# Optimization experiments

Hardware: AMD Instinct MI355X
Metric: run time of the kernel (lower is better)

Reference implementation:

```python
import jax, jax.numpy as jnp
import numpy as np

N = 100000   # nodes
E = 1600000  # edges (avg degree 16)
D = 256      # in_channels == out_channels
EPS = 1e-3   # Keras LayerNormalization default epsilon


def setup_inputs() -> dict:
    key = jax.random.key(0)
    k1, k2, k3 = jax.random.split(key, 3)
    x = jax.random.normal(k1, (N, D), dtype=jnp.float32)
    edge_index = jax.random.randint(k2, (2, E), 0, N, dtype=jnp.int32)
    W = jax.random.normal(k3, (D, D), dtype=jnp.float32) / np.float32(np.sqrt(D))
    b = jnp.zeros((D,), dtype=jnp.float32)
    gamma = jnp.ones((D,), dtype=jnp.float32)
    beta = jnp.zeros((D,), dtype=jnp.float32)
    return {"x": x, "edge_index": edge_index, "W": W, "b": b, "gamma": gamma, "beta": beta}


def reference(x, edge_index, W, b, gamma, beta):
    src, dst = edge_index[0], edge_index[1]
    n = x.shape[0]
    # in-degree with self-loop, symmetric GCN normalization 1/sqrt(d_i d_j)
    deg = jax.ops.segment_sum(jnp.ones((src.shape[0],), x.dtype), dst, num_segments=n) + 1.0
    norm = jax.lax.rsqrt(deg)               # [N]
    h = x @ W                               # [N, D] dense transform
    msg = h[src] * norm[src, None]          # gather + scale, [E, D]
    agg = jax.ops.segment_sum(msg, dst, num_segments=n) * norm[:, None]
    agg = agg + h * (norm * norm)[:, None] + b   # self-loop term + bias
    # residual (in_channels == out_channels) + layer norm
    y = x + agg
    mean = jnp.mean(y, axis=-1, keepdims=True)
    var = jnp.mean(jnp.square(y - mean), axis=-1, keepdims=True)
    return gamma * (y - mean) * jax.lax.rsqrt(var + EPS) + beta
```

## Files before the change

kernel.cpp:

```cpp
#include <hip/hip_runtime.h>


#define D_DIM 256
#define NPART 8
#define SLOTS 64

typedef __attribute__((ext_vector_type(8))) short short8;
typedef __attribute__((ext_vector_type(4))) float f32x4;
typedef __attribute__((ext_vector_type(2))) float f32x2;

__device__ __forceinline__ unsigned short f2bf(float f) {
    unsigned int u = __builtin_bit_cast(unsigned int, f);
    u = (u + 0x7fffu + ((u >> 16) & 1u)) >> 16;
    return (unsigned short)u;
}
__device__ __forceinline__ unsigned int pack2(float a, float b) {
    return (unsigned int)f2bf(a) | ((unsigned int)f2bf(b) << 16);
}

__device__ __forceinline__ unsigned int fp8e(float f) {
    float a = fminf(fmaxf(f, -448.f), 448.f);
    unsigned int u = __builtin_bit_cast(unsigned int, a);
    unsigned int s = (u >> 24) & 0x80u;
    int e = (int)((u >> 23) & 0xffu);
    unsigned int man = u & 0x7fffffu;
    if (e >= 121) {
        unsigned int mant = man >> 20;
        unsigned int rest = man & 0xfffffu;
        unsigned int inc = (rest > 0x80000u) || (rest == 0x80000u && (mant & 1u));
        unsigned int code = (((unsigned int)(e - 120)) << 3) | mant;
        code += inc;
        if (code > 0x7eu) code = 0x7eu;
        return s | code;
    }
    float m = fabsf(a) * 512.f;
    unsigned int mi = (unsigned int)rintf(m);
    return s | mi;
}

__global__ void zero_ints(int* __restrict__ p, int n) {
    int i = blockIdx.x * blockDim.x + threadIdx.x;
    if (i < n) p[i] = 0;
}

__global__ void fill_pad_part(const int* __restrict__ src, const int* __restrict__ dst,
                              int E, int* __restrict__ cnt, int* __restrict__ srcs_pad,
                              int npp) {
    const int part = blockIdx.x & (NPART - 1);
    const int bid  = blockIdx.x >> 3;
    const int nblk = gridDim.x >> 3;
    const int lo = part * npp, hi = lo + npp;
    for (int e = bid * blockDim.x + threadIdx.x; e < E; e += nblk * blockDim.x) {
        int d = dst[e];
        if (d >= lo && d < hi) {
            int pos = atomicAdd(&cnt[d], 1);
            if (pos < SLOTS) srcs_pad[(size_t)d * SLOTS + pos] = src[e];
        }
    }
}

__global__ void make_nrm(const int* __restrict__ cnt, float* __restrict__ nrm, int N) {
    int i = blockIdx.x * blockDim.x + threadIdx.x;
    if (i < N) nrm[i] = rsqrtf((float)cnt[i] + 1.0f);
}

__global__ void cast_wt(const float* __restrict__ W, unsigned short* __restrict__ Wt) {
    int t = blockIdx.x * blockDim.x + threadIdx.x;
    int k = t >> 8, n = t & 255;
    Wt[(size_t)n * D_DIM + k] = f2bf(W[(size_t)k * D_DIM + n]);
}

#define GBM 128
#define LDA 40

__global__ __launch_bounds__(512) void gemm_mfma(
    const float* __restrict__ X, const unsigned short* __restrict__ Wt,
    const float* __restrict__ nrm, unsigned char* __restrict__ Hs8,
    int M, int ntiles) {
    __shared__ unsigned short WtL[256 * 256];
    __shared__ unsigned short As[2][GBM * LDA];

    const int t    = threadIdx.x;
    const int lane = t & 63;
    const int wave = t >> 6;
    const int wr   = wave >> 2, wc = wave & 3;

#pragma unroll
    for (int c = 0; c < 16; ++c) {
        int u  = c * 512 + t;
        int n  = u >> 5;
        int kc = (u & 31) * 8;
        int ks = kc ^ ((n & 15) << 3);
        *(uint4*)&WtL[n * 256 + ks] = *(const uint4*)(Wt + (size_t)n * 256 + kc);
    }

    const int arow = t >> 2;
    const int akc  = (t & 3) * 8;
    const int kp   = (lane >> 4) * 8;

    for (int tile = blockIdx.x; tile < ntiles; tile += gridDim.x) {
        const int m0 = tile * GBM;
        const int xr = (m0 + arow < M) ? (m0 + arow) : (M - 1);
        const float* xp = X + (size_t)xr * D_DIM;

        {
            float4 a0 = *(const float4*)(xp + akc);
            float4 a1 = *(const float4*)(xp + akc + 4);
            uint4 A = {pack2(a0.x, a0.y), pack2(a0.z, a0.w),
                       pack2(a1.x, a1.y), pack2(a1.z, a1.w)};
            *(uint4*)&As[0][arow * LDA + akc] = A;
        }
        __syncthreads();

        f32x4 acc[4][4];
#pragma unroll
        for (int mi = 0; mi < 4; ++mi)
#pragma unroll
            for (int ni = 0; ni < 4; ++ni) acc[mi][ni] = (f32x4){0.f, 0.f, 0.f, 0.f};

        for (int s = 0; s < 8; ++s) {
            float4 a0, a1;
            if (s < 7) {
                a0 = *(const float4*)(xp + (s + 1) * 32 + akc);
                a1 = *(const float4*)(xp + (s + 1) * 32 + akc + 4);
            }

            short8 af[4], bfr[4];
#pragma unroll
            for (int mi = 0; mi < 4; ++mi)
                af[mi] = *(const short8*)&As[s & 1][(wr * 64 + mi * 16 + (lane & 15)) * LDA + kp];
#pragma unroll
            for (int ni = 0; ni < 4; ++ni) {
                int n  = wc * 64 + ni * 16 + (lane & 15);
                int k  = s * 32 + kp;
                int ks = k ^ ((n & 15) << 3);
                bfr[ni] = *(const short8*)&WtL[n * 256 + ks];
            }
#pragma unroll
            for (int mi = 0; mi < 4; ++mi)
#pragma unroll
                for (int ni = 0; ni < 4; ++ni)
                    acc[mi][ni] = __builtin_amdgcn_mfma_f32_16x16x32_bf16(
                        af[mi], bfr[ni], acc[mi][ni], 0, 0, 0);

            if (s < 7) {
                uint4 A = {pack2(a0.x, a0.y), pack2(a0.z, a0.w),
                           pack2(a1.x, a1.y), pack2(a1.z, a1.w)};
                *(uint4*)&As[(s + 1) & 1][arow * LDA + akc] = A;
                __syncthreads();
            }
        }

#pragma unroll
        for (int mi = 0; mi < 4; ++mi) {
#pragma unroll
            for (int r = 0; r < 4; ++r) {
                int row = m0 + wr * 64 + mi * 16 + (lane >> 4) * 4 + r;
                if (row < M) {
                    float nr = nrm[row];
#pragma unroll
                    for (int ni = 0; ni < 4; ++ni) {
                        int col = wc * 64 + ni * 16 + (lane & 15);
                        Hs8[(size_t)row * D_DIM + col] =
                            (unsigned char)fp8e(acc[mi][ni][r] * nr);
                    }
                }
            }
        }
    }
}

__global__ __launch_bounds__(256) void agg_ln(
    const float* __restrict__ X, const unsigned char* __restrict__ Hs8,
    const int* __restrict__ cnt, const int* __restrict__ srcs_pad,
    const float* __restrict__ nrm, const float* __restrict__ bvec,
    const float* __restrict__ gamma, const float* __restrict__ beta,
    float* __restrict__ out, int N) {
    const int wave = (blockIdx.x * blockDim.x + threadIdx.x) >> 6;
    const int lane = threadIdx.x & 63;
    if (wave >= N) return;
    const int i = wave;

    auto ldrow = [&](int s) -> unsigned int {
        return *((const unsigned int*)(Hs8 + (size_t)s * D_DIM) + lane);
    };

    unsigned int hv = ldrow(i);
    f32x2 lo = __builtin_amdgcn_cvt_pk_f32_fp8(hv, false);
    f32x2 hi = __builtin_amdgcn_cvt_pk_f32_fp8(hv, true);
    float ax = lo.x, ay = lo.y, az = hi.x, aw = hi.y;

    auto accum = [&](unsigned int v) {
        f32x2 l = __builtin_amdgcn_cvt_pk_f32_fp8(v, false);
        f32x2 h = __builtin_amdgcn_cvt_pk_f32_fp8(v, true);
        ax += l.x; ay += l.y; az += h.x; aw += h.y;
    };

    const int* sp = srcs_pad + (size_t)i * SLOTS;
    const int ci = min(cnt[i], SLOTS);

    int e = 0;
    for (; e + 8 <= ci; e += 8) {
        int s0 = __builtin_amdgcn_readfirstlane(sp[e]);
        int s1 = __builtin_amdgcn_readfirstlane(sp[e + 1]);
        int s2 = __builtin_amdgcn_readfirstlane(sp[e + 2]);
        int s3 = __builtin_amdgcn_readfirstlane(sp[e + 3]);
        int s4 = __builtin_amdgcn_readfirstlane(sp[e + 4]);
        int s5 = __builtin_amdgcn_readfirstlane(sp[e + 5]);
        int s6 = __builtin_amdgcn_readfirstlane(sp[e + 6]);
        int s7 = __builtin_amdgcn_readfirstlane(sp[e + 7]);
        unsigned int h0 = ldrow(s0), h1 = ldrow(s1), h2 = ldrow(s2), h3 = ldrow(s3);
        unsigned int h4 = ldrow(s4), h5 = ldrow(s5), h6 = ldrow(s6), h7 = ldrow(s7);
        accum(h0); accum(h1); accum(h2); accum(h3);
        accum(h4); accum(h5); accum(h6); accum(h7);
    }
    for (; e + 4 <= ci; e += 4) {
        int s0 = __builtin_amdgcn_readfirstlane(sp[e]);
        int s1 = __builtin_amdgcn_readfirstlane(sp[e + 1]);
        int s2 = __builtin_amdgcn_readfirstlane(sp[e + 2]);
        int s3 = __builtin_amdgcn_readfirstlane(sp[e + 3]);
        unsigned int h0 = ldrow(s0), h1 = ldrow(s1), h2 = ldrow(s2), h3 = ldrow(s3);
        accum(h0); accum(h1); accum(h2); accum(h3);
    }
    for (; e < ci; ++e) accum(ldrow(__builtin_amdgcn_readfirstlane(sp[e])));

    const float ni = nrm[i];
    float4 xv = reinterpret_cast<const float4*>(X)[(size_t)i * 64 + lane];
    float4 bv = reinterpret_cast<const float4*>(bvec)[lane];

    float4 y;
    y.x = xv.x + ax * ni + bv.x;
    y.y = xv.y + ay * ni + bv.y;
    y.z = xv.z + az * ni + bv.z;
    y.w = xv.w + aw * ni + bv.w;

    float s1 = y.x + y.y + y.z + y.w;
    float s2 = y.x * y.x + y.y * y.y + y.z * y.z + y.w * y.w;
#pragma unroll
    for (int off = 32; off > 0; off >>= 1) {
        s1 += __shfl_xor(s1, off);
        s2 += __shfl_xor(s2, off);
    }
    const float mean = s1 * (1.0f / 256.0f);
    const float var  = s2 * (1.0f / 256.0f) - mean * mean;
    const float rstd = rsqrtf(var + 1e-3f);

    float4 gv = reinterpret_cast<const float4*>(gamma)[lane];
    float4 be = reinterpret_cast<const float4*>(beta)[lane];
    float4 o;
    o.x = gv.x * (y.x - mean) * rstd + be.x;
    o.y = gv.y * (y.y - mean) * rstd + be.y;
    o.z = gv.z * (y.z - mean) * rstd + be.z;
    o.w = gv.w * (y.w - mean) * rstd + be.w;
    reinterpret_cast<float4*>(out)[(size_t)i * 64 + lane] = o;
}

extern "C" void kernel_launch(void* const* d_in, const int* in_sizes, int n_in,
                              void* d_out, int out_size, void* d_ws, size_t ws_size,
                              hipStream_t stream) {
    const float* x     = (const float*)d_in[0];
    const int*   ei    = (const int*)d_in[1];
    const float* W     = (const float*)d_in[2];
    const float* bvec  = (const float*)d_in[3];
    const float* gamma = (const float*)d_in[4];
    const float* beta  = (const float*)d_in[5];
    float*       out   = (float*)d_out;

    const int D = in_sizes[3];
    const int N = in_sizes[0] / D;
    const int E = in_sizes[1] / 2;
    const int* src = ei;
    const int* dst = ei + E;

    char* w = (char*)d_ws;
    size_t off = 0;
    auto alloc = [&](size_t bytes) -> void* {
        void* p = w + off;
        off = (off + bytes + 255) & ~(size_t)255;
        return p;
    };
    unsigned char*  Hs8      = (unsigned char*)alloc((size_t)N * D);
    unsigned short* Wt       = (unsigned short*)alloc((size_t)D * D * sizeof(unsigned short));
    float*          nrm      = (float*)alloc((size_t)N * sizeof(float));
    int*            cnt      = (int*)alloc((size_t)N * sizeof(int));
    int*            srcs_pad = (int*)alloc((size_t)N * SLOTS * sizeof(int));
    (void)ws_size;

    const int npp    = (N + NPART - 1) / NPART;
    const int ntiles = (N + GBM - 1) / GBM;

    cast_wt<<<(D * D + 255) / 256, 256, 0, stream>>>(W, Wt);
    zero_ints<<<(N + 255) / 256, 256, 0, stream>>>(cnt, N);
    fill_pad_part<<<2048, 256, 0, stream>>>(src, dst, E, cnt, srcs_pad, npp);
    make_nrm<<<(N + 255) / 256, 256, 0, stream>>>(cnt, nrm, N);

    gemm_mfma<<<256, 512, 0, stream>>>(x, Wt, nrm, Hs8, N, ntiles);

    int nwblocks = (N + 3) / 4;
    agg_ln<<<nwblocks, 256, 0, stream>>>(x, Hs8, cnt, srcs_pad, nrm, bvec,
                                         gamma, beta, out, N);
}
```

Measured before the change: 227.1 us.

## Stream W tiles per k-step in GEMM, fuse prep kernels, deepen gather unroll

The GEMM stops preloading the full 128KB transposed weight into LDS per persistent block. It now double-buffers 32-wide k-slices of both X and W and launches one block per 128-row tile, trading more global W reads for much lower LDS use and higher occupancy. The weight cast and the count zeroing are merged into one prep kernel to save a launch. The aggregation gather loop gains a 16-wide unrolled stage to keep more row loads in flight.

```diff
diff --git a/kernel.cpp b/kernel.cpp
--- a/kernel.cpp
+++ b/kernel.cpp
@@ -38,9 +38,14 @@
     return s | mi;
 }
 
-__global__ void zero_ints(int* __restrict__ p, int n) {
+__global__ void prep(const float* __restrict__ W, unsigned short* __restrict__ Wt,
+                     int* __restrict__ cnt, int N) {
     int i = blockIdx.x * blockDim.x + threadIdx.x;
-    if (i < n) p[i] = 0;
+    if (i < D_DIM * D_DIM) {
+        int k = i >> 8, n = i & 255;
+        Wt[(size_t)n * D_DIM + k] = f2bf(W[(size_t)k * D_DIM + n]);
+    }
+    if (i < N) cnt[i] = 0;
 }
 
 __global__ void fill_pad_part(const int* __restrict__ src, const int* __restrict__ dst,
@@ -64,106 +69,95 @@
     if (i < N) nrm[i] = rsqrtf((float)cnt[i] + 1.0f);
 }
 
-__global__ void cast_wt(const float* __restrict__ W, unsigned short* __restrict__ Wt) {
-    int t = blockIdx.x * blockDim.x + threadIdx.x;
-    int k = t >> 8, n = t & 255;
-    Wt[(size_t)n * D_DIM + k] = f2bf(W[(size_t)k * D_DIM + n]);
-}
-
 #define GBM 128
-#define LDA 40
+#define GBK 32
+#define LDK 40
 
 __global__ __launch_bounds__(512) void gemm_mfma(
     const float* __restrict__ X, const unsigned short* __restrict__ Wt,
-    const float* __restrict__ nrm, unsigned char* __restrict__ Hs8,
-    int M, int ntiles) {
-    __shared__ unsigned short WtL[256 * 256];
-    __shared__ unsigned short As[2][GBM * LDA];
+    const float* __restrict__ nrm, unsigned char* __restrict__ Hs8, int M) {
+    __shared__ unsigned short As[2][GBM * LDK];
+    __shared__ unsigned short Bs[2][D_DIM * LDK];
 
     const int t    = threadIdx.x;
     const int lane = t & 63;
     const int wave = t >> 6;
     const int wr   = wave >> 2, wc = wave & 3;
-
-#pragma unroll
-    for (int c = 0; c < 16; ++c) {
-        int u  = c * 512 + t;
-        int n  = u >> 5;
-        int kc = (u & 31) * 8;
-        int ks = kc ^ ((n & 15) << 3);
-        *(uint4*)&WtL[n * 256 + ks] = *(const uint4*)(Wt + (size_t)n * 256 + kc);
-    }
+    const int m0   = blockIdx.x * GBM;
 
     const int arow = t >> 2;
     const int akc  = (t & 3) * 8;
-    const int kp   = (lane >> 4) * 8;
-
-    for (int tile = blockIdx.x; tile < ntiles; tile += gridDim.x) {
-        const int m0 = tile * GBM;
-        const int xr = (m0 + arow < M) ? (m0 + arow) : (M - 1);
-        const float* xp = X + (size_t)xr * D_DIM;
-
-        {
-            float4 a0 = *(const float4*)(xp + akc);
-            float4 a1 = *(const float4*)(xp + akc + 4);
+    const int xr   = (m0 + arow < M) ? (m0 + arow) : (M - 1);
+    const float* xp = X + (size_t)xr * D_DIM;
+    const int bn0 = t >> 2,           bkc0 = (t & 3) * 8;
+    const int bn1 = (t + 512) >> 2,   bkc1 = ((t + 512) & 3) * 8;
+
+    {
+        float4 a0 = *(const float4*)(xp + akc);
+        float4 a1 = *(const float4*)(xp + akc + 4);
+        uint4 A = {pack2(a0.x, a0.y), pack2(a0.z, a0.w),
+                   pack2(a1.x, a1.y), pack2(a1.z, a1.w)};
+        *(uint4*)&As[0][arow * LDK + akc] = A;
+        *(uint4*)&Bs[0][bn0 * LDK + bkc0] = *(const uint4*)(Wt + (size_t)bn0 * D_DIM + bkc0);
+        *(uint4*)&Bs[0][bn1 * LDK + bkc1] = *(const uint4*)(Wt + (size_t)bn1 * D_DIM + bkc1);
+    }
+    __syncthreads();
+
+    f32x4 acc[4][4];
+#pragma unroll
+    for (int mi = 0; mi < 4; ++mi)
+#pragma unroll
+        for (int ni = 0; ni < 4; ++ni) acc[mi][ni] = (f32x4){0.f, 0.f, 0.f, 0.f};
+
+    const int kp = (lane >> 4) * 8;
+
+    for (int s = 0; s < 8; ++s) {
+        float4 a0, a1;
+        uint4  b0, b1;
+        if (s < 7) {
+            int kk = (s + 1) * GBK;
+            a0 = *(const float4*)(xp + kk + akc);
+            a1 = *(const float4*)(xp + kk + akc + 4);
+            b0 = *(const uint4*)(Wt + (size_t)bn0 * D_DIM + kk + bkc0);
+            b1 = *(const uint4*)(Wt + (size_t)bn1 * D_DIM + kk + bkc1);
+        }
+
+        short8 af[4], bfr[4];
+#pragma unroll
+        for (int mi = 0; mi < 4; ++mi)
+            af[mi] = *(const short8*)&As[s & 1][(wr * 64 + mi * 16 + (lane & 15)) * LDK + kp];
+#pragma unroll
+        for (int ni = 0; ni < 4; ++ni)
+            bfr[ni] = *(const short8*)&Bs[s & 1][(wc * 64 + ni * 16 + (lane & 15)) * LDK + kp];
+#pragma unroll
+        for (int mi = 0; mi < 4; ++mi)
+#pragma unroll
+            for (int ni = 0; ni < 4; ++ni)
+                acc[mi][ni] = __builtin_amdgcn_mfma_f32_16x16x32_bf16(
+                    af[mi], bfr[ni], acc[mi][ni], 0, 0, 0);
+
+        if (s < 7) {
             uint4 A = {pack2(a0.x, a0.y), pack2(a0.z, a0.w),
                        pack2(a1.x, a1.y), pack2(a1.z, a1.w)};
-            *(uint4*)&As[0][arow * LDA + akc] = A;
+            *(uint4*)&As[(s + 1) & 1][arow * LDK + akc] = A;
+            *(uint4*)&Bs[(s + 1) & 1][bn0 * LDK + bkc0] = b0;
+            *(uint4*)&Bs[(s + 1) & 1][bn1 * LDK + bkc1] = b1;
+            __syncthreads();
         }
-        __syncthreads();
-
-        f32x4 acc[4][4];
-#pragma unroll
-        for (int mi = 0; mi < 4; ++mi)
-#pragma unroll
-            for (int ni = 0; ni < 4; ++ni) acc[mi][ni] = (f32x4){0.f, 0.f, 0.f, 0.f};
-
-        for (int s = 0; s < 8; ++s) {
-            float4 a0, a1;
-            if (s < 7) {
-                a0 = *(const float4*)(xp + (s + 1) * 32 + akc);
-                a1 = *(const float4*)(xp + (s + 1) * 32 + akc + 4);
-            }
-
-            short8 af[4], bfr[4];
-#pragma unroll
-            for (int mi = 0; mi < 4; ++mi)
-                af[mi] = *(const short8*)&As[s & 1][(wr * 64 + mi * 16 + (lane & 15)) * LDA + kp];
-#pragma unroll
-            for (int ni = 0; ni < 4; ++ni) {
-                int n  = wc * 64 + ni * 16 + (lane & 15);
-                int k  = s * 32 + kp;
-                int ks = k ^ ((n & 15) << 3);
-                bfr[ni] = *(const short8*)&WtL[n * 256 + ks];
-            }
-#pragma unroll
-            for (int mi = 0; mi < 4; ++mi)
-#pragma unroll
-                for (int ni = 0; ni < 4; ++ni)
-                    acc[mi][ni] = __builtin_amdgcn_mfma_f32_16x16x32_bf16(
-                        af[mi], bfr[ni], acc[mi][ni], 0, 0, 0);
-
-            if (s < 7) {
-                uint4 A = {pack2(a0.x, a0.y), pack2(a0.z, a0.w),
-                           pack2(a1.x, a1.y), pack2(a1.z, a1.w)};
-                *(uint4*)&As[(s + 1) & 1][arow * LDA + akc] = A;
-                __syncthreads();
-            }
-        }
-
-#pragma unroll
-        for (int mi = 0; mi < 4; ++mi) {
-#pragma unroll
-            for (int r = 0; r < 4; ++r) {
-                int row = m0 + wr * 64 + mi * 16 + (lane >> 4) * 4 + r;
-                if (row < M) {
-                    float nr = nrm[row];
-#pragma unroll
-                    for (int ni = 0; ni < 4; ++ni) {
-                        int col = wc * 64 + ni * 16 + (lane & 15);
-                        Hs8[(size_t)row * D_DIM + col] =
-                            (unsigned char)fp8e(acc[mi][ni][r] * nr);
-                    }
+    }
+
+#pragma unroll
+    for (int mi = 0; mi < 4; ++mi) {
+#pragma unroll
+        for (int r = 0; r < 4; ++r) {
+            int row = m0 + wr * 64 + mi * 16 + (lane >> 4) * 4 + r;
+            if (row < M) {
+                float nr = nrm[row];
+#pragma unroll
+                for (int ni = 0; ni < 4; ++ni) {
+                    int col = wc * 64 + ni * 16 + (lane & 15);
+                    Hs8[(size_t)row * D_DIM + col] =
+                        (unsigned char)fp8e(acc[mi][ni][r] * nr);
                 }
             }
         }
@@ -200,27 +194,35 @@
     const int ci = min(cnt[i], SLOTS);
 
     int e = 0;
+    for (; e + 16 <= ci; e += 16) {
+        int ss[16];
+        unsigned int hh[16];
+#pragma unroll
+        for (int j = 0; j < 16; ++j) ss[j] = __builtin_amdgcn_readfirstlane(sp[e + j]);
+#pragma unroll
+        for (int j = 0; j < 16; ++j) hh[j] = ldrow(ss[j]);
+#pragma unroll
+        for (int j = 0; j < 16; ++j) accum(hh[j]);
+    }
     for (; e + 8 <= ci; e += 8) {
-        int s0 = __builtin_amdgcn_readfirstlane(sp[e]);
-        int s1 = __builtin_amdgcn_readfirstlane(sp[e + 1]);
-        int s2 = __builtin_amdgcn_readfirstlane(sp[e + 2]);
-        int s3 = __builtin_amdgcn_readfirstlane(sp[e + 3]);
-        int s4 = __builtin_amdgcn_readfirstlane(sp[e + 4]);
-        int s5 = __builtin_amdgcn_readfirstlane(sp[e + 5]);
-        int s6 = __builtin_amdgcn_readfirstlane(sp[e + 6]);
-        int s7 = __builtin_amdgcn_readfirstlane(sp[e + 7]);
-        unsigned int h0 = ldrow(s0), h1 = ldrow(s1), h2 = ldrow(s2), h3 = ldrow(s3);
-        unsigned int h4 = ldrow(s4), h5 = ldrow(s5), h6 = ldrow(s6), h7 = ldrow(s7);
-        accum(h0); accum(h1); accum(h2); accum(h3);
-        accum(h4); accum(h5); accum(h6); accum(h7);
+        int ss[8];
+        unsigned int hh[8];
+#pragma unroll
+        for (int j = 0; j < 8; ++j) ss[j] = __builtin_amdgcn_readfirstlane(sp[e + j]);
+#pragma unroll
+        for (int j = 0; j < 8; ++j) hh[j] = ldrow(ss[j]);
+#pragma unroll
+        for (int j = 0; j < 8; ++j) accum(hh[j]);
     }
     for (; e + 4 <= ci; e += 4) {
-        int s0 = __builtin_amdgcn_readfirstlane(sp[e]);
-        int s1 = __builtin_amdgcn_readfirstlane(sp[e + 1]);
-        int s2 = __builtin_amdgcn_readfirstlane(sp[e + 2]);
-        int s3 = __builtin_amdgcn_readfirstlane(sp[e + 3]);
-        unsigned int h0 = ldrow(s0), h1 = ldrow(s1), h2 = ldrow(s2), h3 = ldrow(s3);
-        accum(h0); accum(h1); accum(h2); accum(h3);
+        int ss[4];
+        unsigned int hh[4];
+#pragma unroll
+        for (int j = 0; j < 4; ++j) ss[j] = __builtin_amdgcn_readfirstlane(sp[e + j]);
+#pragma unroll
+        for (int j = 0; j < 4; ++j) hh[j] = ldrow(ss[j]);
+#pragma unroll
+        for (int j = 0; j < 4; ++j) accum(hh[j]);
     }
     for (; e < ci; ++e) accum(ldrow(__builtin_amdgcn_readfirstlane(sp[e])));
 
@@ -286,15 +288,13 @@
     int*            srcs_pad = (int*)alloc((size_t)N * SLOTS * sizeof(int));
     (void)ws_size;
 
-    const int npp    = (N + NPART - 1) / NPART;
-    const int ntiles = (N + GBM - 1) / GBM;
-
-    cast_wt<<<(D * D + 255) / 256, 256, 0, stream>>>(W, Wt);
-    zero_ints<<<(N + 255) / 256, 256, 0, stream>>>(cnt, N);
+    const int npp = (N + NPART - 1) / NPART;
+
+    prep<<<(N + 255) / 256, 256, 0, stream>>>(W, Wt, cnt, N);
     fill_pad_part<<<2048, 256, 0, stream>>>(src, dst, E, cnt, srcs_pad, npp);
     make_nrm<<<(N + 255) / 256, 256, 0, stream>>>(cnt, nrm, N);
 
-    gemm_mfma<<<256, 512, 0, stream>>>(x, Wt, nrm, Hs8, N, ntiles);
+    gemm_mfma<<<(N + GBM - 1) / GBM, 512, 0, stream>>>(x, Wt, nrm, Hs8, N);
 
     int nwblocks = (N + 3) / 4;
     agg_ln<<<nwblocks, 256, 0, stream>>>(x, Hs8, cnt, srcs_pad, nrm, bvec,
```

Result: faster. 211.9 us (-6.7%).
